# Performance work log

Measured on AMD Instinct MI355X. Metric: run time of the kernel, lower is better.

## Reference

```python
import jax, jax.numpy as jnp
import numpy as np

FOCUS = 3  # focusing_factor
EPS = 1e-6


def setup_inputs() -> dict:
    key = jax.random.key(0)
    ks = jax.random.split(key, 6)
    B, N, C = 4, 4096, 1024
    s = 0.02
    return {
        "x": jax.random.normal(ks[0], (B, N, C), jnp.float32),
        "w_qkv": jax.random.normal(ks[1], (3 * C, C), jnp.float32) * s,
        "w_proj": jax.random.normal(ks[2], (C, C), jnp.float32) * s,
        "b_proj": jax.random.normal(ks[3], (C,), jnp.float32) * s,
        "w_dwc": jax.random.normal(ks[4], (C, 3), jnp.float32) * s,
        "b_dwc": jax.random.normal(ks[5], (C,), jnp.float32) * s,
    }


def _norm_last(t):
    return t / jnp.sum(t, axis=-1, keepdims=True)


def reference(x, w_qkv, w_proj, b_proj, w_dwc, b_dwc):
    B, N, C = x.shape
    H = 16
    d = C // H
    # qkv projection -> (3, B, H, N, d)
    qkv = jnp.einsum('bnc,oc->bno', x, w_qkv).reshape(B, N, 3, H, d)
    qkv = jnp.transpose(qkv, (2, 0, 3, 1, 4))
    q, k, v = qkv[0], qkv[1], qkv[2]
    # focused kernel feature map: relu -> l1 norm -> power -> renorm
    q = _norm_last(jax.nn.relu(q) + EPS)
    k = _norm_last(jax.nn.relu(k) + EPS)
    q = _norm_last(q ** FOCUS)
    k = _norm_last(k ** FOCUS)
    # linear attention
    kv = jnp.einsum('bhnd,bhne->bhde', k, v)                     # (B,H,d,d)
    z = 1.0 / (jnp.einsum('bhnd,bhd->bhn', q, k.sum(axis=2)) + EPS)
    out = jnp.einsum('bhnd,bhde,bhn->bhne', q, kv, z)            # (B,H,N,d)
    out = jnp.transpose(out, (0, 2, 1, 3)).reshape(B, N, C)
    # depthwise conv1d over sequence, kernel=3, padding=1 (torch layout [C,1,3])
    xp = jnp.pad(out, ((0, 0), (1, 1), (0, 0)))
    conv = (xp[:, 0:N, :] * w_dwc[:, 0]
            + xp[:, 1:N + 1, :] * w_dwc[:, 1]
            + xp[:, 2:N + 2, :] * w_dwc[:, 2]) + b_dwc
    out = out + conv
    # output projection (dropout is identity in eval)
    return jnp.einsum('bnc,oc->bno', out, w_proj) + b_proj
```

## Files before the change

### kernel.cpp

```cpp
#include <hip/hip_runtime.h>
#include <hip/hip_bf16.h>

#define BB 4
#define NN 4096
#define CC 1024
#define HH 16
#define MM (BB*NN)
#define EPSF 1e-6f

typedef _Float16 f16x8 __attribute__((ext_vector_type(8)));
typedef float f32x4 __attribute__((ext_vector_type(4)));

__device__ __forceinline__ void gload_lds16(const void* g, void* l) {
    __builtin_amdgcn_global_load_lds(
        (const __attribute__((address_space(1))) void*)g,
        (__attribute__((address_space(3))) void*)l, 16, 0, 0);
}

__global__ __launch_bounds__(256)
void tofp16_all(const float* __restrict__ x, const float* __restrict__ wq,
                const float* __restrict__ wp, _Float16* __restrict__ xf,
                _Float16* __restrict__ wqf, _Float16* __restrict__ wpf)
{
    int i = blockIdx.x * 256 + threadIdx.x;
    const float* src; _Float16* dst; int off;
    if (i < 4194304)      { src = x;  dst = xf;  off = 0; }
    else if (i < 4980736) { src = wq; dst = wqf; off = 4194304; }
    else                  { src = wp; dst = wpf; off = 4980736; }
    int j = i - off;
    float4 f = ((const float4*)src)[j];
    short4 pk;
    pk.x = __builtin_bit_cast(short, (_Float16)f.x);
    pk.y = __builtin_bit_cast(short, (_Float16)f.y);
    pk.z = __builtin_bit_cast(short, (_Float16)f.z);
    pk.w = __builtin_bit_cast(short, (_Float16)f.w);
    ((short4*)dst)[j] = pk;
}


#define STAGE(BUF, KT) do {                                                          \
    _Pragma("unroll")                                                                \
    for (int j_ = 0; j_ < 2; ++j_) {                                                 \
        gload_lds16(gA[j_] + (KT) * 32, (char*)lds + (BUF) * 32768 + lbase[j_]);     \
        gload_lds16(gB[j_] + (KT) * 32, (char*)lds + (BUF) * 32768 + 16384 + lbase[j_]); \
    } } while (0)

#define TILE(KT, CUR, NXT, DOSTAGE, VMSTR) do {                                      \
    if (DOSTAGE) STAGE(NXT, (KT) + 2);                                               \
    const char* Ab_ = (const char*)lds + (CUR) * 32768 + aoff;                       \
    const char* Bb_ = (const char*)lds + (CUR) * 32768 + 16384 + boff;               \
    f16x8 af_[8], bf_[4];                                                            \
    _Pragma("unroll")                                                                \
    for (int m_ = 0; m_ < 8; ++m_) af_[m_] = *(const f16x8*)(Ab_ + m_ * 1024);       \
    _Pragma("unroll")                                                                \
    for (int n_ = 0; n_ < 4; ++n_) bf_[n_] = *(const f16x8*)(Bb_ + n_ * 1024);       \
    __builtin_amdgcn_s_setprio(1);                                                   \
    _Pragma("unroll")                                                                \
    for (int m_ = 0; m_ < 8; ++m_)                                                   \
    _Pragma("unroll")                                                                \
    for (int n_ = 0; n_ < 4; ++n_)                                                   \
        acc[m_][n_] = __builtin_amdgcn_mfma_f32_16x16x32_f16(af_[m_], bf_[n_],       \
                                                             acc[m_][n_], 0, 0, 0); \
    __builtin_amdgcn_s_setprio(0);                                                   \
    asm volatile("s_waitcnt " VMSTR ::: "memory");                                   \
    __builtin_amdgcn_s_barrier();                                                    \
    __builtin_amdgcn_sched_barrier(0);                                               \
} while (0)

template<int EPI>
__global__ __launch_bounds__(512, 2)
void gemm256(const _Float16* __restrict__ A, const _Float16* __restrict__ Bm,
             void* __restrict__ Cout, _Float16* __restrict__ Kt,
             _Float16* __restrict__ Vt, const float* __restrict__ bias,
             const int Ncols, const int gx)
{
    __shared__ _Float16 lds[3 * 16384];

    const int tid  = threadIdx.x;
    const int lane = tid & 63;
    const int wid  = tid >> 6;
    const int wm   = wid >> 2;
    const int wn   = wid & 3;

    const int nwg = gridDim.x;
    const int wg  = blockIdx.x;
    const int sw  = (wg & 7) * (nwg >> 3) + (wg >> 3);
    const int by  = sw / gx, bx = sw - by * gx;
    const int brow = by << 8, bcol = bx << 8;

    const _Float16* gA[2]; const _Float16* gB[2]; int lbase[2];
#pragma unroll
    for (int j = 0; j < 2; ++j) {
        int pos = ((wid * 2 + j) << 10) + (lane << 4);
        int r   = pos >> 6;
        int c8  = ((pos >> 4) & 3) ^ ((r >> 1) & 3);
        gA[j] = A  + (size_t)(brow + r) * 1024 + c8 * 8;
        gB[j] = Bm + (size_t)(bcol + r) * 1024 + c8 * 8;
        lbase[j] = (wid * 2 + j) << 10;
    }

    const int swz  = (((lane >> 4) ^ ((lane >> 1) & 3)) << 4);
    const int aoff = (wm * 128 + (lane & 15)) * 64 + swz;
    const int boff = (wn * 64  + (lane & 15)) * 64 + swz;

    f32x4 acc[8][4] = {};

    STAGE(0, 0);
    STAGE(1, 1);
    asm volatile("s_waitcnt vmcnt(4)" ::: "memory");
    __builtin_amdgcn_s_barrier();
    __builtin_amdgcn_sched_barrier(0);

#pragma unroll 1
    for (int tt = 0; tt < 30; tt += 3) {
        TILE(tt,     0, 2, 1, "vmcnt(4)");
        TILE(tt + 1, 1, 0, 1, "vmcnt(4)");
        TILE(tt + 2, 2, 1, 1, "vmcnt(4)");
    }
    TILE(30, 0, 2, 0, "vmcnt(0)");
    TILE(31, 1, 0, 0, "vmcnt(0)");

    if (EPI == 0) {
        const int sec = bcol >> 10;
        const bool feat = (sec < 2);
        if (feat) {
#pragma unroll
            for (int m = 0; m < 8; ++m)
#pragma unroll
                for (int r = 0; r < 4; ++r) {
                    float u[4]; float ssum = 0.f;
#pragma unroll
                    for (int n = 0; n < 4; ++n) {
                        float uu = fmaxf(acc[m][n][r], 0.f) + EPSF;
                        float c = uu * uu * uu;
                        u[n] = c; ssum += c;
                    }
                    ssum += __shfl_xor(ssum, 1, 16);
                    ssum += __shfl_xor(ssum, 2, 16);
                    ssum += __shfl_xor(ssum, 4, 16);
                    ssum += __shfl_xor(ssum, 8, 16);
                    float inv = 1.0f / ssum;
#pragma unroll
                    for (int n = 0; n < 4; ++n) acc[m][n][r] = u[n] * inv;
                }
        }
        if (sec == 0) {
            _Float16* Qh = (_Float16*)Cout;
            const int b  = brow >> 12;
            const int h  = (bcol >> 6) + wn;
            const size_t qb = (size_t)(b * 16 + h) * 4096;
            const int n0 = (brow & 4095) + wm * 128;
            const int l15 = lane & 15, q = lane >> 4;
#pragma unroll
            for (int m = 0; m < 8; ++m) {
                int nr = n0 + m * 16 + q * 4;
#pragma unroll
                for (int r = 0; r < 4; ++r) {
                    size_t base = (qb + nr + r) * 64 + l15;
#pragma unroll
                    for (int n = 0; n < 4; ++n)
                        Qh[base + n * 16] = (_Float16)acc[m][n][r];
                }
            }
        } else {
            _Float16* T = (sec == 1) ? Kt : Vt;
            const int b   = brow >> 12;
            const int hb  = ((bcol & 1023) >> 6) + wn;
            const int bh  = b * 16 + hb;
            const int n0  = (brow & 4095) + wm * 128;
            char* st = (char*)lds + wid * 8704;
            const int p = lane & 15, q2 = lane >> 4;
#pragma unroll
            for (int c2 = 0; c2 < 2; ++c2) {
#pragma unroll
                for (int m = 0; m < 4; ++m) {
                    int mm = c2 * 4 + m;
                    int tokc = m * 16 + q2 * 4;
#pragma unroll
                    for (int n = 0; n < 4; ++n) {
                        short4 pk;
                        pk.x = __builtin_bit_cast(short, (_Float16)acc[mm][n][0]);
                        pk.y = __builtin_bit_cast(short, (_Float16)acc[mm][n][1]);
                        pk.z = __builtin_bit_cast(short, (_Float16)acc[mm][n][2]);
                        pk.w = __builtin_bit_cast(short, (_Float16)acc[mm][n][3]);
                        int dk = n * 16 + p;
                        *(short4*)(st + dk * 136 + tokc * 2) = pk;
                    }
                }
#pragma unroll
                for (int it = 0; it < 16; ++it) {
                    int dk = it * 4 + q2;
                    short4 v4 = *(const short4*)(st + dk * 136 + p * 8);
                    *(short4*)(T + ((size_t)(bh * 64 + dk)) * 4096 + n0 + c2 * 64 + p * 4) = v4;
                }
            }
        }
    } else {
        float* Oc = (float*)Cout;
        const int colb = bcol + wn * 64 + (lane & 15);
#pragma unroll
        for (int m = 0; m < 8; ++m) {
            int rb = brow + wm * 128 + m * 16 + (lane >> 4) * 4;
#pragma unroll
            for (int r = 0; r < 4; ++r) {
                size_t base = (size_t)(rb + r) * Ncols + colb;
#pragma unroll
                for (int n = 0; n < 4; ++n)
                    Oc[base + n * 16] = acc[m][n][r] + bias[colb + n * 16];
            }
        }
    }
}

__global__ __launch_bounds__(256)
void kv_mfma(const _Float16* __restrict__ Kt, const _Float16* __restrict__ Vt,
             float* __restrict__ kvp, float* __restrict__ ksump)
{
    __shared__ float red[4][64][64];
    __shared__ float ksr[4][64];
    int bx = blockIdx.x;
    int bh = bx >> 2, kseg = bx & 3;
    int tid = threadIdx.x;
    int w = tid >> 6, lane = tid & 63, p = lane & 15, q = lane >> 4;
    const _Float16* Vb = Vt + (size_t)bh * 64 * 4096;
    const _Float16* Kb = Kt + (size_t)bh * 64 * 4096;
    f32x4 acc[4][4] = {};
    float ksp[4] = {0.f, 0.f, 0.f, 0.f};
    int kbase = kseg * 1024 + w * 256 + q * 8;
#pragma unroll 1
    for (int ks = 0; ks < 8; ++ks) {
        int kb = kbase + ks * 32;
        f16x8 af[4], bf[4];
#pragma unroll
        for (int m = 0; m < 4; ++m)
            af[m] = *(const f16x8*)(Vb + (size_t)(m * 16 + p) * 4096 + kb);
#pragma unroll
        for (int n = 0; n < 4; ++n) {
            bf[n] = *(const f16x8*)(Kb + (size_t)(n * 16 + p) * 4096 + kb);
#pragma unroll
            for (int j = 0; j < 8; ++j) ksp[n] += (float)bf[n][j];
        }
#pragma unroll
        for (int m = 0; m < 4; ++m)
#pragma unroll
            for (int n = 0; n < 4; ++n)
                acc[m][n] = __builtin_amdgcn_mfma_f32_16x16x32_f16(
                    af[m], bf[n], acc[m][n], 0, 0, 0);
    }
#pragma unroll
    for (int n = 0; n < 4; ++n) {
        ksp[n] += __shfl_xor(ksp[n], 16);
        ksp[n] += __shfl_xor(ksp[n], 32);
    }
    if (q == 0)
#pragma unroll
        for (int n = 0; n < 4; ++n) ksr[w][n * 16 + p] = ksp[n];
#pragma unroll
    for (int m = 0; m < 4; ++m)
#pragma unroll
        for (int n = 0; n < 4; ++n)
            *(f32x4*)&red[w][n * 16 + p][m * 16 + q * 4] = acc[m][n];
    __syncthreads();
    int dv = tid & 63, dkb = (tid >> 6) * 16;
    float* ko = kvp + ((size_t)(kseg * 64 + bh)) * 4096;
    f32x4 o[4];
#pragma unroll
    for (int i = 0; i < 16; ++i) {
        float s = red[0][dkb + i][dv] + red[1][dkb + i][dv]
                + red[2][dkb + i][dv] + red[3][dkb + i][dv];
        o[i >> 2][i & 3] = s;
    }
#pragma unroll
    for (int i = 0; i < 4; ++i)
        *(f32x4*)(ko + dv * 64 + dkb + i * 4) = o[i];
    if (tid < 64)
        ksump[(size_t)(kseg * 64 + bh) * 64 + tid] =
            ksr[0][tid] + ksr[1][tid] + ksr[2][tid] + ksr[3][tid];
}

__global__ __launch_bounds__(256)
void kv_reduce(const float* __restrict__ kvp, const float* __restrict__ ksump,
               _Float16* __restrict__ kvT)
{
    int idx = blockIdx.x * 256 + threadIdx.x;
    int col = idx & 63;
    int t = idx >> 6;
    int bh = t / 80;
    int row = t - bh * 80;
    float s = 0.f;
    if (row < 64) {
        int src = bh * 4096 + row * 64 + col;
        s = kvp[src] + kvp[262144 + src] + kvp[2 * 262144 + src] + kvp[3 * 262144 + src];
    } else if (row == 64) {
        int src = bh * 64 + col;
        s = ksump[src] + ksump[4096 + src] + ksump[2 * 4096 + src] + ksump[3 * 4096 + src];
    }
    kvT[idx] = (_Float16)s;
}

__global__ __launch_bounds__(256)
void attn_conv(const _Float16* __restrict__ Qh, const _Float16* __restrict__ kvT,
               const float* __restrict__ wdwc, const float* __restrict__ bdwc,
               _Float16* __restrict__ yf)
{
    __shared__ _Float16 ybuf[258][68];
    int blk = blockIdx.x;
    int b = blk >> 8, h = (blk >> 4) & 15, chunk = blk & 15;
    int bh = b * 16 + h;
    int tid = threadIdx.x, w = tid >> 6, lane = tid & 63, p = lane & 15, q = lane >> 4;
    const _Float16* kvb = kvT + (size_t)bh * (80 * 64);
    const _Float16* Qb  = Qh + (size_t)bh * 4096 * 64;
    f16x8 bf[2][5];
#pragma unroll
    for (int kst = 0; kst < 2; ++kst)
#pragma unroll
        for (int n = 0; n < 5; ++n)
            bf[kst][n] = *(const f16x8*)(kvb + (n * 16 + p) * 64 + kst * 32 + q * 8);

    int tok0 = chunk * 256 + w * 64;

    f32x4 acc[4][5] = {};
#pragma unroll
    for (int kst = 0; kst < 2; ++kst) {
        f16x8 af[4];
#pragma unroll
        for (int m = 0; m < 4; ++m)
            af[m] = *(const f16x8*)(Qb + (size_t)(tok0 + m * 16 + p) * 64 + kst * 32 + q * 8);
#pragma unroll
        for (int m = 0; m < 4; ++m)
#pragma unroll
            for (int n = 0; n < 5; ++n)
                acc[m][n] = __builtin_amdgcn_mfma_f32_16x16x32_f16(
                    af[m], bf[kst][n], acc[m][n], 0, 0, 0);
    }
#pragma unroll
    for (int m = 0; m < 4; ++m)
#pragma unroll
        for (int r = 0; r < 4; ++r) {
            float sz = __shfl(acc[m][4][r], lane & 48);
            float zz = 1.0f / (sz + EPSF);
            int row = 1 + w * 64 + m * 16 + q * 4 + r;
#pragma unroll
            for (int n = 0; n < 4; ++n)
                ybuf[row][n * 16 + p] = (_Float16)(acc[m][n][r] * zz);
        }
    if (w == 0) {
        float val = 0.f;
        if (chunk > 0) {
            int t = chunk * 256 - 1;
            float sd = 0.f, sz = 0.f;
#pragma unroll
            for (int i = 0; i < 8; ++i) {
                f16x8 qq = *(const f16x8*)(Qb + (size_t)t * 64 + i * 8);
                f16x8 kk = *(const f16x8*)(kvb + lane * 64 + i * 8);
                f16x8 ks = *(const f16x8*)(kvb + 64 * 64 + i * 8);
#pragma unroll
                for (int j = 0; j < 8; ++j) {
                    sd += (float)qq[j] * (float)kk[j];
                    sz += (float)qq[j] * (float)ks[j];
                }
            }
            val = sd / (sz + EPSF);
        }
        ybuf[0][lane] = (_Float16)val;
    }
    if (w == 3) {
        float val = 0.f;
        if (chunk < 15) {
            int t = chunk * 256 + 256;
            float sd = 0.f, sz = 0.f;
#pragma unroll
            for (int i = 0; i < 8; ++i) {
                f16x8 qq = *(const f16x8*)(Qb + (size_t)t * 64 + i * 8);
                f16x8 kk = *(const f16x8*)(kvb + lane * 64 + i * 8);
                f16x8 ks = *(const f16x8*)(kvb + 64 * 64 + i * 8);
#pragma unroll
                for (int j = 0; j < 8; ++j) {
                    sd += (float)qq[j] * (float)kk[j];
                    sz += (float)qq[j] * (float)ks[j];
                }
            }
            val = sd / (sz + EPSF);
        }
        ybuf[257][lane] = (_Float16)val;
    }
    __syncthreads();
    int dv = lane;
    int c = h * 64 + dv;
    float w0 = wdwc[c * 3 + 0], w1 = wdwc[c * 3 + 1], w2 = wdwc[c * 3 + 2];
    float bb = bdwc[c];
#pragma unroll 4
    for (int it = 0; it < 64; ++it) {
        int tok = it * 4 + w;
        float ym = (float)ybuf[tok][dv];
        float yc = (float)ybuf[tok + 1][dv];
        float yp = (float)ybuf[tok + 2][dv];
        float val = yc + w0 * ym + w1 * yc + w2 * yp + bb;
        yf[((size_t)(b * 4096 + chunk * 256 + tok)) * 1024 + c] = (_Float16)val;
    }
}

extern "C" void kernel_launch(void* const* d_in, const int* in_sizes, int n_in,
                              void* d_out, int out_size, void* d_ws, size_t ws_size,
                              hipStream_t stream)
{
    const float* x      = (const float*)d_in[0];
    const float* w_qkv  = (const float*)d_in[1];
    const float* w_proj = (const float*)d_in[2];
    const float* b_proj = (const float*)d_in[3];
    const float* w_dwc  = (const float*)d_in[4];
    const float* b_dwc  = (const float*)d_in[5];

    char* p = (char*)d_ws;
    _Float16* xf   = (_Float16*)p;  p += (size_t)MM * CC * 2;
    _Float16* wqf  = (_Float16*)p;  p += (size_t)3 * CC * CC * 2;
    _Float16* wpf  = (_Float16*)p;  p += (size_t)CC * CC * 2;
    _Float16* Qh   = (_Float16*)p;  p += (size_t)MM * CC * 2;
    _Float16* Kt   = (_Float16*)p;  p += (size_t)64 * 64 * NN * 2;
    _Float16* Vt   = (_Float16*)p;  p += (size_t)64 * 64 * NN * 2;
    float*    kvp  = (float*)p;     p += (size_t)4 * 64 * 4096 * 4;
    float*    ksump= (float*)p;     p += (size_t)4 * 64 * 64 * 4;
    _Float16* kvT  = (_Float16*)p;  p += (size_t)64 * 80 * 64 * 2;
    _Float16* yf   = (_Float16*)p;  p += (size_t)MM * CC * 2;

    tofp16_all<<<20480, 256, 0, stream>>>(x, w_qkv, w_proj, xf, wqf, wpf);

    gemm256<0><<<dim3(12 * 64), 512, 0, stream>>>(
        xf, wqf, (void*)Qh, Kt, Vt, nullptr, 3072, 12);

    kv_mfma<<<256, 256, 0, stream>>>(Kt, Vt, kvp, ksump);
    kv_reduce<<<1280, 256, 0, stream>>>(kvp, ksump, kvT);

    attn_conv<<<BB * HH * 16, 256, 0, stream>>>(Qh, kvT, w_dwc, b_dwc, yf);

    gemm256<1><<<dim3(4 * 64), 512, 0, stream>>>(
        yf, wpf, d_out, nullptr, nullptr, b_proj, 1024, 4);
}
```

Baseline: 218.3 us.

## Load B operand directly from global into registers, staging only A in LDS

The GEMM kernel now stages only the A tile through LDS with a triple buffer, while each wave loads its B fragments straight from global memory into double-buffered registers one k-step ahead. This halves LDS footprint and LDS read traffic per tile, which may raise occupancy and cut LDS bandwidth pressure. The cost is uncoalesced-ish global B loads duplicated across the two wm waves and more VGPRs for the prefetch buffers. The attention-conv halo computation for waves 0 and 3 is also merged into one code path.

```diff
diff --git a/kernel.cpp b/kernel.cpp
--- a/kernel.cpp
+++ b/kernel.cpp
@@ -38,28 +38,29 @@
 }
 
 
-#define STAGE(BUF, KT) do {                                                          \
+#define STAGE_A(BUF, KT) do {                                                        \
     _Pragma("unroll")                                                                \
-    for (int j_ = 0; j_ < 2; ++j_) {                                                 \
-        gload_lds16(gA[j_] + (KT) * 32, (char*)lds + (BUF) * 32768 + lbase[j_]);     \
-        gload_lds16(gB[j_] + (KT) * 32, (char*)lds + (BUF) * 32768 + 16384 + lbase[j_]); \
-    } } while (0)
-
-#define TILE(KT, CUR, NXT, DOSTAGE, VMSTR) do {                                      \
-    if (DOSTAGE) STAGE(NXT, (KT) + 2);                                               \
-    const char* Ab_ = (const char*)lds + (CUR) * 32768 + aoff;                       \
-    const char* Bb_ = (const char*)lds + (CUR) * 32768 + 16384 + boff;               \
-    f16x8 af_[8], bf_[4];                                                            \
+    for (int j_ = 0; j_ < 2; ++j_)                                                   \
+        gload_lds16(gA[j_] + (KT) * 32, (char*)lds + (BUF) * 16384 + lbase[j_]);     \
+} while (0)
+
+#define TILEB(KT, CUR, NXT, BCUR, BNXT, DOB, DOSTAGE, VMSTR) do {                    \
+    if (DOB) {                                                                       \
+        _Pragma("unroll")                                                            \
+        for (int n_ = 0; n_ < 4; ++n_)                                               \
+            BNXT[n_] = *(const f16x8*)(gBF[n_] + ((KT) + 1) * 32);                   \
+    }                                                                                \
+    if (DOSTAGE) STAGE_A(NXT, (KT) + 2);                                             \
+    const char* Ab_ = (const char*)lds + (CUR) * 16384 + aoff;                       \
+    f16x8 af_[8];                                                                    \
     _Pragma("unroll")                                                                \
     for (int m_ = 0; m_ < 8; ++m_) af_[m_] = *(const f16x8*)(Ab_ + m_ * 1024);       \
-    _Pragma("unroll")                                                                \
-    for (int n_ = 0; n_ < 4; ++n_) bf_[n_] = *(const f16x8*)(Bb_ + n_ * 1024);       \
     __builtin_amdgcn_s_setprio(1);                                                   \
     _Pragma("unroll")                                                                \
     for (int m_ = 0; m_ < 8; ++m_)                                                   \
     _Pragma("unroll")                                                                \
     for (int n_ = 0; n_ < 4; ++n_)                                                   \
-        acc[m_][n_] = __builtin_amdgcn_mfma_f32_16x16x32_f16(af_[m_], bf_[n_],       \
+        acc[m_][n_] = __builtin_amdgcn_mfma_f32_16x16x32_f16(af_[m_], BCUR[n_],      \
                                                              acc[m_][n_], 0, 0, 0); \
     __builtin_amdgcn_s_setprio(0);                                                   \
     asm volatile("s_waitcnt " VMSTR ::: "memory");                                   \
@@ -69,12 +70,12 @@
 
 template<int EPI>
 __global__ __launch_bounds__(512, 2)
-void gemm256(const _Float16* __restrict__ A, const _Float16* __restrict__ Bm,
-             void* __restrict__ Cout, _Float16* __restrict__ Kt,
-             _Float16* __restrict__ Vt, const float* __restrict__ bias,
-             const int Ncols, const int gx)
-{
-    __shared__ _Float16 lds[3 * 16384];
+void gemmBD(const _Float16* __restrict__ A, const _Float16* __restrict__ Bm,
+            void* __restrict__ Cout, _Float16* __restrict__ Kt,
+            _Float16* __restrict__ Vt, const float* __restrict__ bias,
+            const int Ncols, const int gx)
+{
+    __shared__ _Float16 lds[36864];
 
     const int tid  = threadIdx.x;
     const int lane = tid & 63;
@@ -88,37 +89,49 @@
     const int by  = sw / gx, bx = sw - by * gx;
     const int brow = by << 8, bcol = bx << 8;
 
-    const _Float16* gA[2]; const _Float16* gB[2]; int lbase[2];
+    const _Float16* gA[2]; int lbase[2];
 #pragma unroll
     for (int j = 0; j < 2; ++j) {
         int pos = ((wid * 2 + j) << 10) + (lane << 4);
         int r   = pos >> 6;
         int c8  = ((pos >> 4) & 3) ^ ((r >> 1) & 3);
-        gA[j] = A  + (size_t)(brow + r) * 1024 + c8 * 8;
-        gB[j] = Bm + (size_t)(bcol + r) * 1024 + c8 * 8;
+        gA[j] = A + (size_t)(brow + r) * 1024 + c8 * 8;
         lbase[j] = (wid * 2 + j) << 10;
     }
 
-    const int swz  = (((lane >> 4) ^ ((lane >> 1) & 3)) << 4);
-    const int aoff = (wm * 128 + (lane & 15)) * 64 + swz;
-    const int boff = (wn * 64  + (lane & 15)) * 64 + swz;
+    const int l15 = lane & 15, q = lane >> 4;
+    const int swz  = ((q ^ ((l15 >> 1) & 3)) << 4);
+    const int aoff = (wm * 128 + l15) * 64 + swz;
+
+    const _Float16* gBF[4];
+#pragma unroll
+    for (int n = 0; n < 4; ++n)
+        gBF[n] = Bm + (size_t)(bcol + wn * 64 + n * 16 + l15) * 1024 + q * 8;
 
     f32x4 acc[8][4] = {};
-
-    STAGE(0, 0);
-    STAGE(1, 1);
-    asm volatile("s_waitcnt vmcnt(4)" ::: "memory");
+    f16x8 bb0[4], bb1[4];
+
+    STAGE_A(0, 0);
+    __builtin_amdgcn_sched_barrier(0);
+#pragma unroll
+    for (int n = 0; n < 4; ++n) bb0[n] = *(const f16x8*)(gBF[n]);
+    __builtin_amdgcn_sched_barrier(0);
+    STAGE_A(1, 1);
+    asm volatile("s_waitcnt vmcnt(6)" ::: "memory");
     __builtin_amdgcn_s_barrier();
     __builtin_amdgcn_sched_barrier(0);
 
 #pragma unroll 1
-    for (int tt = 0; tt < 30; tt += 3) {
-        TILE(tt,     0, 2, 1, "vmcnt(4)");
-        TILE(tt + 1, 1, 0, 1, "vmcnt(4)");
-        TILE(tt + 2, 2, 1, 1, "vmcnt(4)");
-    }
-    TILE(30, 0, 2, 0, "vmcnt(0)");
-    TILE(31, 1, 0, 0, "vmcnt(0)");
+    for (int tt = 0; tt < 30; tt += 6) {
+        TILEB(tt + 0, 0, 2, bb0, bb1, 1, 1, "vmcnt(6)");
+        TILEB(tt + 1, 1, 0, bb1, bb0, 1, 1, "vmcnt(6)");
+        TILEB(tt + 2, 2, 1, bb0, bb1, 1, 1, "vmcnt(6)");
+        TILEB(tt + 3, 0, 2, bb1, bb0, 1, 1, "vmcnt(6)");
+        TILEB(tt + 4, 1, 0, bb0, bb1, 1, 1, "vmcnt(6)");
+        TILEB(tt + 5, 2, 1, bb1, bb0, 1, 1, "vmcnt(6)");
+    }
+    TILEB(30, 0, 2, bb0, bb1, 1, 0, "vmcnt(4)");
+    TILEB(31, 1, 0, bb1, bb0, 0, 0, "vmcnt(0)");
 
     if (EPI == 0) {
         const int sec = bcol >> 10;
@@ -150,7 +163,6 @@
             const int h  = (bcol >> 6) + wn;
             const size_t qb = (size_t)(b * 16 + h) * 4096;
             const int n0 = (brow & 4095) + wm * 128;
-            const int l15 = lane & 15, q = lane >> 4;
 #pragma unroll
             for (int m = 0; m < 8; ++m) {
                 int nr = n0 + m * 16 + q * 4;
@@ -169,13 +181,12 @@
             const int bh  = b * 16 + hb;
             const int n0  = (brow & 4095) + wm * 128;
             char* st = (char*)lds + wid * 8704;
-            const int p = lane & 15, q2 = lane >> 4;
 #pragma unroll
             for (int c2 = 0; c2 < 2; ++c2) {
 #pragma unroll
                 for (int m = 0; m < 4; ++m) {
                     int mm = c2 * 4 + m;
-                    int tokc = m * 16 + q2 * 4;
+                    int tokc = m * 16 + q * 4;
 #pragma unroll
                     for (int n = 0; n < 4; ++n) {
                         short4 pk;
@@ -183,24 +194,24 @@
                         pk.y = __builtin_bit_cast(short, (_Float16)acc[mm][n][1]);
                         pk.z = __builtin_bit_cast(short, (_Float16)acc[mm][n][2]);
                         pk.w = __builtin_bit_cast(short, (_Float16)acc[mm][n][3]);
-                        int dk = n * 16 + p;
+                        int dk = n * 16 + l15;
                         *(short4*)(st + dk * 136 + tokc * 2) = pk;
                     }
                 }
 #pragma unroll
                 for (int it = 0; it < 16; ++it) {
-                    int dk = it * 4 + q2;
-                    short4 v4 = *(const short4*)(st + dk * 136 + p * 8);
-                    *(short4*)(T + ((size_t)(bh * 64 + dk)) * 4096 + n0 + c2 * 64 + p * 4) = v4;
+                    int dk = it * 4 + q;
+                    short4 v4 = *(const short4*)(st + dk * 136 + l15 * 8);
+                    *(short4*)(T + ((size_t)(bh * 64 + dk)) * 4096 + n0 + c2 * 64 + l15 * 4) = v4;
                 }
             }
         }
     } else {
         float* Oc = (float*)Cout;
-        const int colb = bcol + wn * 64 + (lane & 15);
+        const int colb = bcol + wn * 64 + l15;
 #pragma unroll
         for (int m = 0; m < 8; ++m) {
-            int rb = brow + wm * 128 + m * 16 + (lane >> 4) * 4;
+            int rb = brow + wm * 128 + m * 16 + q * 4;
 #pragma unroll
             for (int r = 0; r < 4; ++r) {
                 size_t base = (size_t)(rb + r) * Ncols + colb;
@@ -344,10 +355,12 @@
             for (int n = 0; n < 4; ++n)
                 ybuf[row][n * 16 + p] = (_Float16)(acc[m][n][r] * zz);
         }
-    if (w == 0) {
+    if (w == 0 || w == 3) {
+        bool lo = (w == 0);
+        bool live = lo ? (chunk > 0) : (chunk < 15);
         float val = 0.f;
-        if (chunk > 0) {
-            int t = chunk * 256 - 1;
+        if (live) {
+            int t = lo ? (chunk * 256 - 1) : (chunk * 256 + 256);
             float sd = 0.f, sz = 0.f;
 #pragma unroll
             for (int i = 0; i < 8; ++i) {
@@ -362,27 +375,7 @@
             }
             val = sd / (sz + EPSF);
         }
-        ybuf[0][lane] = (_Float16)val;
-    }
-    if (w == 3) {
-        float val = 0.f;
-        if (chunk < 15) {
-            int t = chunk * 256 + 256;
-            float sd = 0.f, sz = 0.f;
-#pragma unroll
-            for (int i = 0; i < 8; ++i) {
-                f16x8 qq = *(const f16x8*)(Qb + (size_t)t * 64 + i * 8);
-                f16x8 kk = *(const f16x8*)(kvb + lane * 64 + i * 8);
-                f16x8 ks = *(const f16x8*)(kvb + 64 * 64 + i * 8);
-#pragma unroll
-                for (int j = 0; j < 8; ++j) {
-                    sd += (float)qq[j] * (float)kk[j];
-                    sz += (float)qq[j] * (float)ks[j];
-                }
-            }
-            val = sd / (sz + EPSF);
-        }
-        ybuf[257][lane] = (_Float16)val;
+        ybuf[lo ? 0 : 257][lane] = (_Float16)val;
     }
     __syncthreads();
     int dv = lane;
@@ -425,7 +418,7 @@
 
     tofp16_all<<<20480, 256, 0, stream>>>(x, w_qkv, w_proj, xf, wqf, wpf);
 
-    gemm256<0><<<dim3(12 * 64), 512, 0, stream>>>(
+    gemmBD<0><<<dim3(12 * 64), 512, 0, stream>>>(
         xf, wqf, (void*)Qh, Kt, Vt, nullptr, 3072, 12);
 
     kv_mfma<<<256, 256, 0, stream>>>(Kt, Vt, kvp, ksump);
@@ -433,6 +426,6 @@
 
     attn_conv<<<BB * HH * 16, 256, 0, stream>>>(Qh, kvT, w_dwc, b_dwc, yf);
 
-    gemm256<1><<<dim3(4 * 64), 512, 0, stream>>>(
+    gemmBD<1><<<dim3(4 * 64), 512, 0, stream>>>(
         yf, wpf, d_out, nullptr, nullptr, b_proj, 1024, 4);
 }
```

Result: slower. 274.4 us (+25.7%).
